# Kernel optimization log

Hardware: AMD Instinct MI355X
Metric: run time of the kernel (lower is better)

The kernel has to match this reference:

```python
import jax, jax.numpy as jnp
import numpy as np

NHID = 128
NLAYERS = 4
DT = 1.0
ALPHA = 1.0
GAMMA = 1.0


def setup_inputs() -> dict:
    key = jax.random.key(0)
    k1, k2, k3, k4, k5, k6 = jax.random.split(key, 6)
    N, E = 100000, 1600000
    stdv = 1.0 / np.sqrt(NHID)
    x = jax.random.normal(k1, (N, NHID), dtype=jnp.float32)
    edge_index = jax.random.randint(k2, (2, E), 0, N, dtype=jnp.int64)
    # GCNConv.lin weight (no bias) and separate conv bias; reset_params uniform(-stdv, stdv) for weights
    W = jax.random.uniform(k3, (NHID, NHID), jnp.float32, -stdv, stdv)
    b = jnp.zeros((NHID,), jnp.float32)
    Wres = jax.random.uniform(k4, (NHID, NHID), jnp.float32, -stdv, stdv)
    bres = jax.random.uniform(k5, (NHID,), jnp.float32, -stdv, stdv)
    return {"x": x, "edge_index": edge_index, "W": W, "b": b, "Wres": Wres, "bres": bres}


def reference(x, edge_index, W, b, Wres, bres):
    N = x.shape[0]
    src, dst = edge_index[0], edge_index[1]
    # GCN degree normalization with self-loops (A_hat = A + I)
    deg = jax.ops.segment_sum(jnp.ones(src.shape[0], x.dtype), dst, num_segments=N) + 1.0
    dinv = jax.lax.rsqrt(deg)  # deg >= 1 from self-loops

    def conv(X):
        h = X @ W  # lin (no bias)
        norm = (dinv[src] * dinv[dst])[:, None]
        msg = h[src] * norm                      # [E, nhid] gather
        agg = jax.ops.segment_sum(msg, dst, num_segments=N)  # scatter-add
        agg = agg + h * (dinv * dinv)[:, None]   # self-loop contribution
        return agg + b

    def residual(X):
        # res_connection_v1: -res(conv.lin(X))
        return -((X @ W) @ Wres + bres)

    # dropout is identity in eval mode
    Y = jnp.tanh(x)
    X = Y
    for _ in range(NLAYERS):
        Y = Y + DT * (jnp.tanh(conv(X) + residual(X)) - ALPHA * Y - GAMMA * X)
        X = X + DT * Y
    return X
```

## Files before the change

### kernel.cpp

```cpp
#include <hip/hip_runtime.h>
#include <hip/hip_bf16.h>
#include <stdint.h>

#define THREADS 256
#define WB 256
#define MAXNB 512
#define NBLK_A 512
#define ECAP 64

typedef unsigned short u16;
typedef unsigned int u32;
using frag_ab = __attribute__((ext_vector_type(8))) short;
using f32x4  = __attribute__((ext_vector_type(4))) float;

static __host__ __device__ inline int imin(int a, int b) { return a < b ? a : b; }

static __device__ inline u16 f2b(float f) {
    u32 u = __builtin_bit_cast(u32, f);
    return (u16)((u + 0x7FFFu + ((u >> 16) & 1u)) >> 16);
}
static __device__ inline float b2f_lo(u32 v) { return __builtin_bit_cast(float, v << 16); }
static __device__ inline float b2f_hi(u32 v) { return __builtin_bit_cast(float, v & 0xFFFF0000u); }

static __device__ inline float tanh_fast(float x) {
    const float e = __builtin_amdgcn_exp2f(x * 2.8853900817779268f);
    return 1.0f - 2.0f * __builtin_amdgcn_rcpf(e + 1.0f);
}

static __device__ inline void fma8(float* a, float w, uint4 v) {
    a[0] = fmaf(w, b2f_lo(v.x), a[0]); a[1] = fmaf(w, b2f_hi(v.x), a[1]);
    a[2] = fmaf(w, b2f_lo(v.y), a[2]); a[3] = fmaf(w, b2f_hi(v.y), a[3]);
    a[4] = fmaf(w, b2f_lo(v.z), a[4]); a[5] = fmaf(w, b2f_hi(v.z), a[5]);
    a[6] = fmaf(w, b2f_lo(v.w), a[6]); a[7] = fmaf(w, b2f_hi(v.w), a[7]);
}

static __device__ inline bool detect64(const int* raw) {
    __shared__ int s64;
    if (threadIdx.x == 0) s64 = 1;
    __syncthreads();
    if (raw[2 * threadIdx.x + 1] != 0) s64 = 0;
    __syncthreads();
    return s64 != 0;
}

__global__ __launch_bounds__(256)
void k_bucket_count(const int* __restrict__ raw, int E, int EPB, int NB,
                    int* __restrict__ counts) {
    const bool is64 = detect64(raw);
    __shared__ int cnt[MAXNB];
    const int t = threadIdx.x, blk = blockIdx.x;
    for (int i = t; i < NB; i += THREADS) cnt[i] = 0;
    __syncthreads();
    const int e0 = blk * EPB, e1 = imin(E, e0 + EPB);
    for (int e = e0 + t; e < e1; e += THREADS) {
        const int d = is64 ? raw[2 * E + 2 * e] : raw[E + e];
        atomicAdd(&cnt[d >> 8], 1);
    }
    __syncthreads();
    for (int i = t; i < NB; i += THREADS) counts[i * NBLK_A + blk] = cnt[i];
}

__global__ void k_chunk_sums(const int* __restrict__ a, int* __restrict__ chunkSum, int L) {
    __shared__ int sm[THREADS];
    const int base = blockIdx.x * 2048 + threadIdx.x * 8;
    int s = 0;
#pragma unroll
    for (int i = 0; i < 8; ++i) { int idx = base + i; if (idx < L) s += a[idx]; }
    sm[threadIdx.x] = s;
    __syncthreads();
    for (int off = THREADS / 2; off > 0; off >>= 1) {
        if (threadIdx.x < off) sm[threadIdx.x] += sm[threadIdx.x + off];
        __syncthreads();
    }
    if (threadIdx.x == 0) chunkSum[blockIdx.x] = sm[0];
}

__global__ void k_scan_offsets(const int* __restrict__ chunkSum, int* __restrict__ chunkOff,
                               int nChunks) {
    if (blockIdx.x == 0 && threadIdx.x == 0) {
        int run = 0;
        for (int i = 0; i < nChunks; ++i) { chunkOff[i] = run; run += chunkSum[i]; }
    }
}

__global__ void k_scan_write(int* __restrict__ a, const int* __restrict__ chunkOff, int L) {
    __shared__ int sm[THREADS];
    const int tid = threadIdx.x;
    const int base = blockIdx.x * 2048 + tid * 8;
    int v[8]; int s = 0;
#pragma unroll
    for (int i = 0; i < 8; ++i) { int idx = base + i; v[i] = (idx < L) ? a[idx] : 0; s += v[i]; }
    const int mysum = s;
    sm[tid] = s;
    __syncthreads();
    for (int off = 1; off < THREADS; off <<= 1) {
        int t = (tid >= off) ? sm[tid - off] : 0;
        __syncthreads();
        sm[tid] += t;
        __syncthreads();
    }
    int run = chunkOff[blockIdx.x] + sm[tid] - mysum;
#pragma unroll
    for (int i = 0; i < 8; ++i) {
        int idx = base + i;
        if (idx < L) { a[idx] = run; run += v[i]; }
    }
}

__global__ __launch_bounds__(256)
void k_bucket_scatter(const int* __restrict__ raw, int E, int EPB, int NB,
                      const int* __restrict__ offs, u32* __restrict__ pairs) {
    const bool is64 = detect64(raw);
    __shared__ int cur[MAXNB];
    const int t = threadIdx.x, blk = blockIdx.x;
    for (int i = t; i < NB; i += THREADS) cur[i] = offs[i * NBLK_A + blk];
    __syncthreads();
    const int e0 = blk * EPB, e1 = imin(E, e0 + EPB);
    for (int e = e0 + t; e < e1; e += THREADS) {
        int s, d;
        if (is64) { s = raw[2 * e]; d = raw[2 * E + 2 * e]; }
        else      { s = raw[e];     d = raw[E + e]; }
        const int p = atomicAdd(&cur[d >> 8], 1);
        pairs[p] = (u32)s | ((u32)(d & 255) << 24);
    }
}

__global__ __launch_bounds__(256)
void k_build(const u32* __restrict__ pairs, const int* __restrict__ offs,
             int* __restrict__ rowptr, int* __restrict__ csr_src,
             float* __restrict__ dinv, int N, int NB, int E) {
    __shared__ int deg[WB];
    __shared__ int ptr[WB];
    __shared__ int cur[WB];
    const int k = blockIdx.x, t = threadIdx.x;
    const int base = offs[k * NBLK_A];
    const int end  = (k + 1 < NB) ? offs[(k + 1) * NBLK_A] : E;
    const int n0 = k * WB;
    deg[t] = 0;
    __syncthreads();
    for (int e = base + t; e < end; e += THREADS)
        atomicAdd(&deg[pairs[e] >> 24], 1);
    __syncthreads();
    const int dv = deg[t];
    if (n0 + t < N) dinv[n0 + t] = rsqrtf((float)dv + 1.0f);
    ptr[t] = dv;
    __syncthreads();
    for (int off = 1; off < THREADS; off <<= 1) {
        int v = (t >= off) ? ptr[t - off] : 0;
        __syncthreads();
        ptr[t] += v;
        __syncthreads();
    }
    const int excl = ptr[t] - dv;
    if (n0 + t < N) rowptr[n0 + t] = base + excl;
    if (k == NB - 1 && t == 0) rowptr[N] = E;
    cur[t] = base + excl;
    __syncthreads();
    for (int e = base + t; e < end; e += THREADS) {
        const u32 w = pairs[e];
        const int p = atomicAdd(&cur[w >> 24], 1);
        csr_src[p] = (int)(w & 0xFFFFFF);
    }
}

__global__ void k_wfill(const int* __restrict__ csr_src, const float* __restrict__ dinv,
                        uint2* __restrict__ csrW, int E) {
    int i = blockIdx.x * blockDim.x + threadIdx.x;
    const int st = gridDim.x * blockDim.x;
    for (; i < E; i += st) {
        const int s = csr_src[i];
        csrW[i] = make_uint2((u32)s, __builtin_bit_cast(u32, dinv[s]));
    }
}

__global__ void k_w2(const float* __restrict__ W, const float* __restrict__ Wres,
                     const float* __restrict__ b, const float* __restrict__ bres,
                     u16* __restrict__ Bt, float* __restrict__ cvec) {
    const int gid = blockIdx.x * blockDim.x + threadIdx.x;
    if (gid < 128 * 128) {
        const int i = gid >> 7, n = gid & 127;
        float s = 0.f;
#pragma unroll 8
        for (int k = 0; k < 128; ++k) s += W[i * 128 + k] * Wres[k * 128 + n];
        Bt[n * 256 + 128 + i] = f2b(-s);
        Bt[n * 256 + i]       = f2b(W[i * 128 + n]);
    }
    if (gid < 128) cvec[gid] = b[gid] - bres[gid];
}

__global__ void k_tanh0(const float* __restrict__ x, u16* __restrict__ Xh, long long n4) {
    long long i = blockIdx.x * (long long)blockDim.x + threadIdx.x;
    const long long stride = gridDim.x * (long long)blockDim.x;
    for (; i < n4; i += stride) {
        float4 v = ((const float4*)x)[i];
        u32 lo = f2b(tanh_fast(v.x)) | ((u32)f2b(tanh_fast(v.y)) << 16);
        u32 hi = f2b(tanh_fast(v.z)) | ((u32)f2b(tanh_fast(v.w)) << 16);
        ((uint2*)Xh)[i] = make_uint2(lo, hi);
    }
}

__global__ __launch_bounds__(256)
void k_agg(const u16* __restrict__ Xh, const int* __restrict__ rowptr,
           const uint2* __restrict__ csrW, u16* __restrict__ Ph, int N) {
    __shared__ uint2 cws[16][ECAP];
    const int qid = threadIdx.x >> 4;
    const int l16 = threadIdx.x & 15;
    const int node = blockIdx.x * 16 + qid;
    const bool valid = node < N;
    const int c8 = l16 * 8;
    int e0 = 0, e1 = 0;
    if (valid) { e0 = rowptr[node]; e1 = rowptr[node + 1]; }
    const int deg = e1 - e0;
    const int ns = deg < ECAP ? deg : ECAP;
    for (int j = l16; j < ns; j += 16)
        cws[qid][j] = csrW[e0 + j];
    const float dn = rsqrtf((float)deg + 1.0f);
    float acc[8] = {0.f, 0.f, 0.f, 0.f, 0.f, 0.f, 0.f, 0.f};
    if (valid) {
        const uint4 v = *(const uint4*)&Xh[(size_t)node * 128 + c8];
        fma8(acc, dn, v);
    }
    int j = 0;
    for (; j + 3 < ns; j += 4) {
        const uint2 cw0 = cws[qid][j],     cw1 = cws[qid][j + 1];
        const uint2 cw2 = cws[qid][j + 2], cw3 = cws[qid][j + 3];
        const uint4 v0 = *(const uint4*)&Xh[(size_t)cw0.x * 128 + c8];
        const uint4 v1 = *(const uint4*)&Xh[(size_t)cw1.x * 128 + c8];
        const uint4 v2 = *(const uint4*)&Xh[(size_t)cw2.x * 128 + c8];
        const uint4 v3 = *(const uint4*)&Xh[(size_t)cw3.x * 128 + c8];
        fma8(acc, __builtin_bit_cast(float, cw0.y), v0);
        fma8(acc, __builtin_bit_cast(float, cw1.y), v1);
        fma8(acc, __builtin_bit_cast(float, cw2.y), v2);
        fma8(acc, __builtin_bit_cast(float, cw3.y), v3);
    }
    for (; j < ns; ++j) {
        const uint2 cw = cws[qid][j];
        const uint4 v = *(const uint4*)&Xh[(size_t)cw.x * 128 + c8];
        fma8(acc, __builtin_bit_cast(float, cw.y), v);
    }
    for (int e = e0 + ECAP; e < e1; ++e) {
        const uint2 cw = csrW[e];
        const uint4 v = *(const uint4*)&Xh[(size_t)cw.x * 128 + c8];
        fma8(acc, __builtin_bit_cast(float, cw.y), v);
    }
    if (valid) {
        u32 w0 = (u32)f2b(acc[0] * dn) | ((u32)f2b(acc[1] * dn) << 16);
        u32 w1 = (u32)f2b(acc[2] * dn) | ((u32)f2b(acc[3] * dn) << 16);
        u32 w2 = (u32)f2b(acc[4] * dn) | ((u32)f2b(acc[5] * dn) << 16);
        u32 w3 = (u32)f2b(acc[6] * dn) | ((u32)f2b(acc[7] * dn) << 16);
        *(uint4*)&Ph[(size_t)node * 128 + c8] = make_uint4(w0, w1, w2, w3);
    }
}

__global__ __launch_bounds__(256)
void k_gemm_mfma(const u16* __restrict__ Ph, const u16* __restrict__ Xh,
                 const u16* __restrict__ Bt, const float* __restrict__ cvec,
                 float* __restrict__ Xout, u16* __restrict__ XhOut, int M, int writeF32) {
    __shared__ u16 Bs[128 * 128];
    const int tid = threadIdx.x;
    const int wid = tid >> 6, lane = tid & 63;
    const int rowbase = blockIdx.x * 128 + wid * 32;
    const int rl = lane & 15;
    const int kg = (lane >> 4) * 8;

    const int r0 = rowbase + rl;
    const size_t ar0 = (size_t)((r0      < M) ? r0      : M - 1);
    const size_t ar1 = (size_t)((r0 + 16 < M) ? r0 + 16 : M - 1);

    frag_ab a0[8], a1[8];
#pragma unroll
    for (int ks = 0; ks < 4; ++ks) {
        const int kk = ks * 32 + kg;
        a0[ks]     = *(const frag_ab*)&Ph[ar0 * 128 + kk];
        a1[ks]     = *(const frag_ab*)&Ph[ar1 * 128 + kk];
        a0[ks + 4] = *(const frag_ab*)&Xh[ar0 * 128 + kk];
        a1[ks + 4] = *(const frag_ab*)&Xh[ar1 * 128 + kk];
    }

    f32x4 acc[2][8];
#pragma unroll
    for (int i = 0; i < 2; ++i)
#pragma unroll
        for (int j = 0; j < 8; ++j) acc[i][j] = (f32x4){0.f, 0.f, 0.f, 0.f};

#pragma unroll
    for (int half = 0; half < 2; ++half) {
#pragma unroll
        for (int p = 0; p < 8; ++p) {
            const int c = p * 256 + tid;
            const int row = c >> 4, c16 = c & 15;
            const uint4 v = *(const uint4*)&Bt[row * 256 + half * 128 + c16 * 8];
            *(uint4*)&Bs[row * 128 + (((c16 * 16) ^ ((row & 7) << 4)) >> 1)] = v;
        }
        __syncthreads();
#pragma unroll
        for (int ks = 0; ks < 4; ++ks) {
            const int kb = ks * 64 + kg * 2;
#pragma unroll
            for (int nf = 0; nf < 8; ++nf) {
                const int r = nf * 16 + rl;
                const frag_ab bv = *(const frag_ab*)&Bs[r * 128 + ((kb ^ ((r & 7) << 4)) >> 1)];
                acc[0][nf] = __builtin_amdgcn_mfma_f32_16x16x32_bf16(a0[half * 4 + ks], bv,
                                                                      acc[0][nf], 0, 0, 0);
                acc[1][nf] = __builtin_amdgcn_mfma_f32_16x16x32_bf16(a1[half * 4 + ks], bv,
                                                                      acc[1][nf], 0, 0, 0);
            }
        }
        __syncthreads();
    }

    const int rq = (lane >> 4) * 4;
    if (writeF32) {
#pragma unroll
        for (int mf = 0; mf < 2; ++mf)
#pragma unroll
            for (int nf = 0; nf < 8; ++nf) {
                const int c = nf * 16 + rl;
                const float cv = cvec[c];
#pragma unroll
                for (int reg = 0; reg < 4; ++reg) {
                    const int r = rowbase + mf * 16 + rq + reg;
                    if (r < M) Xout[(size_t)r * 128 + c] = tanh_fast(acc[mf][nf][reg] + cv);
                }
            }
    } else {
#pragma unroll
        for (int mf = 0; mf < 2; ++mf)
#pragma unroll
            for (int nf = 0; nf < 8; ++nf) {
                const int c = nf * 16 + rl;
                const float cv = cvec[c];
#pragma unroll
                for (int reg = 0; reg < 4; ++reg) {
                    const int rloc = wid * 32 + mf * 16 + rq + reg;
                    Bs[rloc * 128 + (c ^ ((rloc & 7) << 3))] =
                        f2b(tanh_fast(acc[mf][nf][reg] + cv));
                }
            }
        __syncthreads();
#pragma unroll
        for (int k = 0; k < 8; ++k) {
            const int ci = k * 256 + tid;
            const int row = ci >> 4, c8 = ci & 15;
            const int gr = blockIdx.x * 128 + row;
            if (gr < M) {
                const uint4 v = *(const uint4*)&Bs[row * 128 + ((c8 * 8) ^ ((row & 7) << 3))];
                *(uint4*)&XhOut[(size_t)gr * 128 + c8 * 8] = v;
            }
        }
    }
}

extern "C" void kernel_launch(void* const* d_in, const int* in_sizes, int n_in,
                              void* d_out, int out_size, void* d_ws, size_t ws_size,
                              hipStream_t stream) {
    const float* x    = (const float*)d_in[0];
    const int*   ei   = (const int*)d_in[1];
    const float* W    = (const float*)d_in[2];
    const float* b    = (const float*)d_in[3];
    const float* Wres = (const float*)d_in[4];
    const float* bres = (const float*)d_in[5];
    const int N = in_sizes[0] / 128;
    const int E = in_sizes[1] / 2;
    float* X = (float*)d_out;

    uint8_t* base = (uint8_t*)d_ws;
    size_t off = 0;
    auto carve = [&](size_t bytes) -> void* {
        void* p = base + off;
        off += (bytes + 255) & ~(size_t)255;
        return p;
    };
    const int NB = imin((N + WB - 1) / WB, MAXNB);
    const int L = NB * NBLK_A;

    u16*   Xh       = (u16*)carve((size_t)N * 128 * sizeof(u16));
    u16*   Ph       = (u16*)carve((size_t)N * 128 * sizeof(u16));
    u32*   pairs    = (u32*)carve((size_t)E * sizeof(u32));
    uint2* csrW     = (uint2*)carve((size_t)E * sizeof(uint2));
    int*   csr_src  = (int*)carve((size_t)E * sizeof(int));
    int*   counts   = (int*)carve((size_t)L * sizeof(int));
    int*   rowptr   = (int*)carve(((size_t)N + 1) * sizeof(int));
    float* dinv     = (float*)carve((size_t)N * sizeof(float));
    u16*   Bt       = (u16*)carve(128 * 256 * sizeof(u16));
    float* cvec     = (float*)carve(128 * sizeof(float));
    int*   chunkSum = (int*)carve(4096);
    int*   chunkOff = (int*)carve(4096);

    const int EPB = (E + NBLK_A - 1) / NBLK_A;
    const int nChunks = (L + 2047) / 2048;

    k_bucket_count<<<NBLK_A, THREADS, 0, stream>>>(ei, E, EPB, NB, counts);
    k_chunk_sums<<<nChunks, THREADS, 0, stream>>>(counts, chunkSum, L);
    k_scan_offsets<<<1, 64, 0, stream>>>(chunkSum, chunkOff, nChunks);
    k_scan_write<<<nChunks, THREADS, 0, stream>>>(counts, chunkOff, L);
    k_bucket_scatter<<<NBLK_A, THREADS, 0, stream>>>(ei, E, EPB, NB, counts, pairs);
    k_build<<<NB, THREADS, 0, stream>>>(pairs, counts, rowptr, csr_src, dinv, N, NB, E);
    k_wfill<<<2048, THREADS, 0, stream>>>(csr_src, dinv, csrW, E);
    k_w2<<<64, THREADS, 0, stream>>>(W, Wres, b, bres, Bt, cvec);

    const long long n4 = (long long)N * 32;
    const int tgrid = imin((int)((n4 + THREADS - 1) / THREADS), 2048);
    k_tanh0<<<tgrid, THREADS, 0, stream>>>(x, Xh, n4);

    for (int l = 0; l < 4; ++l) {
        k_agg<<<(N + 15) / 16, THREADS, 0, stream>>>(Xh, rowptr, csrW, Ph, N);
        k_gemm_mfma<<<(N + 127) / 128, THREADS, 0, stream>>>(Ph, Xh, Bt, cvec, X, Xh, N,
                                                             (l == 3) ? 1 : 0);
    }
}
```

Measured before the change: 419.2 us.

## Pre-swizzle weights, load B via global_load_lds, fuse wfill and tanh kernels

The weight-prep kernel now writes Bt already in the XOR-swizzled LDS layout. The GEMM can then copy each B half straight into shared memory with global_load_lds instead of staging it through registers. The GEMM also loads the Xh A-fragments only after the first half has been computed, which lowers peak register use. Separately, the CSR weight-fill kernel and the initial tanh kernel are merged into one launch that splits its blocks between the two jobs. This saves a launch and lets the two run concurrently, at the cost of relying on global_load_lds semantics and on the layouts matching.

```diff
diff --git a/kernel.cpp b/kernel.cpp
--- a/kernel.cpp
+++ b/kernel.cpp
@@ -163,13 +163,26 @@
     }
 }
 
-__global__ void k_wfill(const int* __restrict__ csr_src, const float* __restrict__ dinv,
-                        uint2* __restrict__ csrW, int E) {
-    int i = blockIdx.x * blockDim.x + threadIdx.x;
-    const int st = gridDim.x * blockDim.x;
-    for (; i < E; i += st) {
-        const int s = csr_src[i];
-        csrW[i] = make_uint2((u32)s, __builtin_bit_cast(u32, dinv[s]));
+__global__ void k_wfill_tanh(const int* __restrict__ csr_src, const float* __restrict__ dinv,
+                             uint2* __restrict__ csrW, int E,
+                             const float* __restrict__ x, u16* __restrict__ Xh,
+                             long long n4, int WFB) {
+    if ((int)blockIdx.x < WFB) {
+        int i = blockIdx.x * blockDim.x + threadIdx.x;
+        const int st = WFB * blockDim.x;
+        for (; i < E; i += st) {
+            const int s = csr_src[i];
+            csrW[i] = make_uint2((u32)s, __builtin_bit_cast(u32, dinv[s]));
+        }
+    } else {
+        long long i = (long long)(blockIdx.x - WFB) * blockDim.x + threadIdx.x;
+        const long long st = (long long)(gridDim.x - WFB) * blockDim.x;
+        for (; i < n4; i += st) {
+            float4 v = ((const float4*)x)[i];
+            u32 lo = f2b(tanh_fast(v.x)) | ((u32)f2b(tanh_fast(v.y)) << 16);
+            u32 hi = f2b(tanh_fast(v.z)) | ((u32)f2b(tanh_fast(v.w)) << 16);
+            ((uint2*)Xh)[i] = make_uint2(lo, hi);
+        }
     }
 }
 
@@ -182,21 +195,13 @@
         float s = 0.f;
 #pragma unroll 8
         for (int k = 0; k < 128; ++k) s += W[i * 128 + k] * Wres[k * 128 + n];
-        Bt[n * 256 + 128 + i] = f2b(-s);
-        Bt[n * 256 + i]       = f2b(W[i * 128 + n]);
+        char* base = (char*)Bt;
+        const int bh = i * 2;
+        const int sb = ((bh & ~15) ^ ((n & 7) << 4)) | (bh & 15);
+        *(u16*)(base + n * 512 + 256 + sb) = f2b(-s);
+        *(u16*)(base + n * 512 + sb)       = f2b(W[i * 128 + n]);
     }
     if (gid < 128) cvec[gid] = b[gid] - bres[gid];
-}
-
-__global__ void k_tanh0(const float* __restrict__ x, u16* __restrict__ Xh, long long n4) {
-    long long i = blockIdx.x * (long long)blockDim.x + threadIdx.x;
-    const long long stride = gridDim.x * (long long)blockDim.x;
-    for (; i < n4; i += stride) {
-        float4 v = ((const float4*)x)[i];
-        u32 lo = f2b(tanh_fast(v.x)) | ((u32)f2b(tanh_fast(v.y)) << 16);
-        u32 hi = f2b(tanh_fast(v.z)) | ((u32)f2b(tanh_fast(v.w)) << 16);
-        ((uint2*)Xh)[i] = make_uint2(lo, hi);
-    }
 }
 
 __global__ __launch_bounds__(256)
@@ -267,14 +272,23 @@
     const size_t ar0 = (size_t)((r0      < M) ? r0      : M - 1);
     const size_t ar1 = (size_t)((r0 + 16 < M) ? r0 + 16 : M - 1);
 
-    frag_ab a0[8], a1[8];
+#pragma unroll
+    for (int p = 0; p < 8; ++p) {
+        const int c = p * 256 + tid;
+        const int row = c >> 4, c16 = c & 15;
+        const char* src = (const char*)Bt + row * 512 + c16 * 16;
+        __builtin_amdgcn_global_load_lds(
+            (const __attribute__((address_space(1))) unsigned int*)(const void*)src,
+            (__attribute__((address_space(3))) unsigned int*)(void*)((char*)Bs + c * 16),
+            16, 0, 0);
+    }
+
+    frag_ab pa0[4], pa1[4];
 #pragma unroll
     for (int ks = 0; ks < 4; ++ks) {
         const int kk = ks * 32 + kg;
-        a0[ks]     = *(const frag_ab*)&Ph[ar0 * 128 + kk];
-        a1[ks]     = *(const frag_ab*)&Ph[ar1 * 128 + kk];
-        a0[ks + 4] = *(const frag_ab*)&Xh[ar0 * 128 + kk];
-        a1[ks + 4] = *(const frag_ab*)&Xh[ar1 * 128 + kk];
+        pa0[ks] = *(const frag_ab*)&Ph[ar0 * 128 + kk];
+        pa1[ks] = *(const frag_ab*)&Ph[ar1 * 128 + kk];
     }
 
     f32x4 acc[2][8];
@@ -283,31 +297,50 @@
 #pragma unroll
         for (int j = 0; j < 8; ++j) acc[i][j] = (f32x4){0.f, 0.f, 0.f, 0.f};
 
-#pragma unroll
-    for (int half = 0; half < 2; ++half) {
-#pragma unroll
-        for (int p = 0; p < 8; ++p) {
-            const int c = p * 256 + tid;
-            const int row = c >> 4, c16 = c & 15;
-            const uint4 v = *(const uint4*)&Bt[row * 256 + half * 128 + c16 * 8];
-            *(uint4*)&Bs[row * 128 + (((c16 * 16) ^ ((row & 7) << 4)) >> 1)] = v;
+    __syncthreads();
+#pragma unroll
+    for (int ks = 0; ks < 4; ++ks) {
+        const int kb = ks * 64 + kg * 2;
+#pragma unroll
+        for (int nf = 0; nf < 8; ++nf) {
+            const int r = nf * 16 + rl;
+            const frag_ab bv = *(const frag_ab*)&Bs[r * 128 + ((kb ^ ((r & 7) << 4)) >> 1)];
+            acc[0][nf] = __builtin_amdgcn_mfma_f32_16x16x32_bf16(pa0[ks], bv, acc[0][nf], 0, 0, 0);
+            acc[1][nf] = __builtin_amdgcn_mfma_f32_16x16x32_bf16(pa1[ks], bv, acc[1][nf], 0, 0, 0);
         }
-        __syncthreads();
-#pragma unroll
-        for (int ks = 0; ks < 4; ++ks) {
-            const int kb = ks * 64 + kg * 2;
-#pragma unroll
-            for (int nf = 0; nf < 8; ++nf) {
-                const int r = nf * 16 + rl;
-                const frag_ab bv = *(const frag_ab*)&Bs[r * 128 + ((kb ^ ((r & 7) << 4)) >> 1)];
-                acc[0][nf] = __builtin_amdgcn_mfma_f32_16x16x32_bf16(a0[half * 4 + ks], bv,
-                                                                      acc[0][nf], 0, 0, 0);
-                acc[1][nf] = __builtin_amdgcn_mfma_f32_16x16x32_bf16(a1[half * 4 + ks], bv,
-                                                                      acc[1][nf], 0, 0, 0);
-            }
+    }
+    __syncthreads();
+
+#pragma unroll
+    for (int p = 0; p < 8; ++p) {
+        const int c = p * 256 + tid;
+        const int row = c >> 4, c16 = c & 15;
+        const char* src = (const char*)Bt + row * 512 + 256 + c16 * 16;
+        __builtin_amdgcn_global_load_lds(
+            (const __attribute__((address_space(1))) unsigned int*)(const void*)src,
+            (__attribute__((address_space(3))) unsigned int*)(void*)((char*)Bs + c * 16),
+            16, 0, 0);
+    }
+    frag_ab xa0[4], xa1[4];
+#pragma unroll
+    for (int ks = 0; ks < 4; ++ks) {
+        const int kk = ks * 32 + kg;
+        xa0[ks] = *(const frag_ab*)&Xh[ar0 * 128 + kk];
+        xa1[ks] = *(const frag_ab*)&Xh[ar1 * 128 + kk];
+    }
+    __syncthreads();
+#pragma unroll
+    for (int ks = 0; ks < 4; ++ks) {
+        const int kb = ks * 64 + kg * 2;
+#pragma unroll
+        for (int nf = 0; nf < 8; ++nf) {
+            const int r = nf * 16 + rl;
+            const frag_ab bv = *(const frag_ab*)&Bs[r * 128 + ((kb ^ ((r & 7) << 4)) >> 1)];
+            acc[0][nf] = __builtin_amdgcn_mfma_f32_16x16x32_bf16(xa0[ks], bv, acc[0][nf], 0, 0, 0);
+            acc[1][nf] = __builtin_amdgcn_mfma_f32_16x16x32_bf16(xa1[ks], bv, acc[1][nf], 0, 0, 0);
         }
-        __syncthreads();
-    }
+    }
+    __syncthreads();
 
     const int rq = (lane >> 4) * 4;
     if (writeF32) {
@@ -396,12 +429,10 @@
     k_scan_write<<<nChunks, THREADS, 0, stream>>>(counts, chunkOff, L);
     k_bucket_scatter<<<NBLK_A, THREADS, 0, stream>>>(ei, E, EPB, NB, counts, pairs);
     k_build<<<NB, THREADS, 0, stream>>>(pairs, counts, rowptr, csr_src, dinv, N, NB, E);
-    k_wfill<<<2048, THREADS, 0, stream>>>(csr_src, dinv, csrW, E);
     k_w2<<<64, THREADS, 0, stream>>>(W, Wres, b, bres, Bt, cvec);
 
     const long long n4 = (long long)N * 32;
-    const int tgrid = imin((int)((n4 + THREADS - 1) / THREADS), 2048);
-    k_tanh0<<<tgrid, THREADS, 0, stream>>>(x, Xh, n4);
+    k_wfill_tanh<<<4096, THREADS, 0, stream>>>(csr_src, dinv, csrW, E, x, Xh, n4, 2048);
 
     for (int l = 0; l < 4; ++l) {
         k_agg<<<(N + 15) / 16, THREADS, 0, stream>>>(Xh, rowptr, csrW, Ph, N);
```

Result: no change. 413.9 us (-1.3%).
